# Optimization experiments

Hardware: AMD Instinct MI355X
Metric: run time of the kernel (lower is better)

The kernel has to match this reference:

```python
import jax, jax.numpy as jnp
import numpy as np

WIN = 8
SHIFT = WIN // 2  # shift=True
NH = 12
HD = 32
EPS = 1e-5


def _rel_pos_index(w):
    coords = np.stack(np.meshgrid(np.arange(w), np.arange(w), indexing='ij')).reshape(2, -1)
    rel = (coords[:, :, None] - coords[:, None, :]).transpose(1, 2, 0)
    rel[..., 0] += w - 1
    rel[..., 1] += w - 1
    rel[..., 0] *= 2 * w - 1
    return rel.sum(-1)  # [w*w, w*w]

REL_IDX = jnp.asarray(_rel_pos_index(WIN), dtype=jnp.int32)


def _ln(x, g, b):
    mu = jnp.mean(x, axis=-1, keepdims=True)
    var = jnp.mean(jnp.square(x - mu), axis=-1, keepdims=True)
    return (x - mu) * jax.lax.rsqrt(var + EPS) * g + b


def setup_inputs() -> dict:
    key = jax.random.key(0)
    ks = jax.random.split(key, 8)
    B, Hh, Ww, C = 16, 64, 64, 384
    s = lambda fan: 1.0 / np.sqrt(fan)
    return {
        'x': jax.random.normal(ks[0], (B, Hh * Ww, C), jnp.float32),
        'norm1_g': jnp.ones((C,), jnp.float32),
        'norm1_b': jnp.zeros((C,), jnp.float32),
        'qkv_w': jax.random.normal(ks[1], (3 * C, C), jnp.float32) * s(C),
        'qkv_b': jnp.zeros((3 * C,), jnp.float32),
        'proj_w': jax.random.normal(ks[2], (C, C), jnp.float32) * s(C),
        'proj_b': jnp.zeros((C,), jnp.float32),
        'rpb_table': jax.random.normal(ks[3], ((2 * WIN - 1) ** 2, NH), jnp.float32) * 0.02,
        'norm2_g': jnp.ones((C,), jnp.float32),
        'norm2_b': jnp.zeros((C,), jnp.float32),
        'fc1_w': jax.random.normal(ks[4], (4 * C, C), jnp.float32) * s(C),
        'fc1_b': jnp.zeros((4 * C,), jnp.float32),
        'fc2_w': jax.random.normal(ks[5], (C, 4 * C), jnp.float32) * s(4 * C),
        'fc2_b': jnp.zeros((C,), jnp.float32),
        'H': Hh,
        'W': Ww,
    }


def reference(x, norm1_g, norm1_b, qkv_w, qkv_b, proj_w, proj_b, rpb_table,
              norm2_g, norm2_b, fc1_w, fc1_b, fc2_w, fc2_b, H, W):
    B, N, C = x.shape
    Nw = WIN * WIN
    shortcut = x
    h = _ln(x, norm1_g, norm1_b)

    # window partition with roll (shifted windows)
    h = h.reshape(B, H, W, C)
    h = jnp.roll(h, shift=(-SHIFT, -SHIFT), axis=(1, 2))
    h = h.reshape(B, H // WIN, WIN, W // WIN, WIN, C).transpose(0, 1, 3, 2, 4, 5)
    h = h.reshape(-1, Nw, C)  # [B*nW, 64, C]

    # window attention
    qkv = h @ qkv_w.T + qkv_b  # [Bw, Nw, 3C]
    qkv = qkv.reshape(-1, Nw, 3, NH, HD).transpose(2, 0, 3, 1, 4)
    q, k, v = qkv[0], qkv[1], qkv[2]  # [Bw, NH, Nw, HD]
    attn = jnp.einsum('bhqd,bhkd->bhqk', q, k) * (HD ** -0.5)
    bias = rpb_table[REL_IDX.reshape(-1)].reshape(Nw, Nw, NH).transpose(2, 0, 1)
    attn = jax.nn.softmax(attn + bias[None], axis=-1)
    o = jnp.einsum('bhqk,bhkd->bhqd', attn, v)
    o = o.transpose(0, 2, 1, 3).reshape(-1, Nw, C)
    o = o @ proj_w.T + proj_b

    # window reverse with inverse roll
    o = o.reshape(B, H // WIN, W // WIN, WIN, WIN, C).transpose(0, 1, 3, 2, 4, 5)
    o = o.reshape(B, H, W, C)
    o = jnp.roll(o, shift=(SHIFT, SHIFT), axis=(1, 2)).reshape(B, N, C)

    x = shortcut + o
    m = _ln(x, norm2_g, norm2_b)
    m = jax.nn.gelu(m @ fc1_w.T + fc1_b, approximate=False)
    m = m @ fc2_w.T + fc2_b
    return x + m
```

## Files before the change

kernel.cpp:

```cpp
#include <hip/hip_runtime.h>
#include <hip/hip_bf16.h>
#include <math.h>

typedef __attribute__((ext_vector_type(8))) short bf16x8;
typedef __attribute__((ext_vector_type(4))) float f32x4;
typedef unsigned short u16;

#define NHEAD 12

__device__ __forceinline__ u16 f2bf(float f) {
  __hip_bfloat16 h = __float2bfloat16(f);
  return __builtin_bit_cast(u16, h);
}

__device__ __forceinline__ void gload16(const void* g, void* l) {
  __builtin_amdgcn_global_load_lds(
      (const __attribute__((address_space(1))) void*)g,
      (__attribute__((address_space(3))) void*)l, 16, 0, 0);
}

__global__ void cvt_all(const float* __restrict__ s0, const float* __restrict__ s1,
                        const float* __restrict__ s2, const float* __restrict__ s3,
                        u16* __restrict__ d) {
  int i = blockIdx.x * 256 + threadIdx.x;
  if (i >= 1769472) return;
  float v;
  if (i < 442368) v = s0[i];
  else if (i < 589824) v = s1[i - 442368];
  else if (i < 1179648) v = s2[i - 589824];
  else v = s3[i - 1179648];
  d[i] = f2bf(v);
}

__global__ void build_bias(const float* __restrict__ rpb, float* __restrict__ bt) {
  int i = blockIdx.x * 256 + threadIdx.x;
  if (i >= NHEAD * 4096) return;
  int h = i >> 12;
  int q = (i >> 6) & 63;
  int k = i & 63;
  int qi = q >> 3, qj = q & 7, ki = k >> 3, kj = k & 7;
  int idx = (qi - ki + 7) * 15 + (qj - kj + 7);
  bt[i] = rpb[idx * NHEAD + h];
}

__global__ __launch_bounds__(256) void ln_k(const float* __restrict__ x,
                                            const float* __restrict__ g,
                                            const float* __restrict__ b,
                                            u16* __restrict__ out) {
  int row = (blockIdx.x << 2) + (threadIdx.x >> 6);
  int lane = threadIdx.x & 63;
  const float* xr = x + (size_t)row * 384;
  float v[6];
  float s = 0.f;
#pragma unroll
  for (int i = 0; i < 6; ++i) { v[i] = xr[lane + (i << 6)]; s += v[i]; }
#pragma unroll
  for (int o = 32; o; o >>= 1) s += __shfl_xor(s, o, 64);
  float mu = s * (1.f / 384.f);
  float vs = 0.f;
#pragma unroll
  for (int i = 0; i < 6; ++i) { float d0 = v[i] - mu; vs += d0 * d0; }
#pragma unroll
  for (int o = 32; o; o >>= 1) vs += __shfl_xor(vs, o, 64);
  float rs = rsqrtf(vs * (1.f / 384.f) + 1e-5f);
  u16* orow = out + (size_t)row * 384;
#pragma unroll
  for (int i = 0; i < 6; ++i) {
    int c = lane + (i << 6);
    orow[c] = f2bf((v[i] - mu) * rs * g[c] + b[c]);
  }
}

template <int EP>
__global__ __launch_bounds__(256, 4) void gemmA(const u16* __restrict__ A,
                                                const u16* __restrict__ W,
                                                const float* __restrict__ bias,
                                                const float* __restrict__ res,
                                                void* __restrict__ outp,
                                                int N, int K, int nCol) {
  __shared__ u16 As[128 * 64];
  __shared__ u16 Bs[128 * 64];
  const int tid = threadIdx.x;
  const int wave = tid >> 6, lane = tid & 63;
  const int wm = wave >> 1, wn = wave & 1;
  const int nwg = gridDim.x, cpx = nwg >> 3;
  const int lin = (blockIdx.x & 7) * cpx + (blockIdx.x >> 3);
  const int rowT = lin / nCol;
  const int colT = lin - rowT * nCol;
  const int rowBase = rowT << 7;
  const int colBase = colT << 7;
  const int nK = K >> 6;

  const int g16 = (tid & 7) ^ ((tid >> 3) & 7);
  const u16* Asrc = A + (size_t)(rowBase + (tid >> 3)) * K + (g16 << 3);
  const u16* Wsrc = W + (size_t)(colBase + (tid >> 3)) * K + (g16 << 3);
  const int ldst = tid << 3;

  const int q4 = lane >> 4;
  const int rx = lane & 7;
  const int arow = (wm << 6) + (lane & 15);
  const int brow = (wn << 6) + (lane & 15);

  f32x4 acc[4][4] = {};

  for (int j = 0; j < nK; ++j) {
    const size_t k0 = (size_t)j << 6;
#pragma unroll
    for (int c = 0; c < 4; ++c) {
      gload16(Asrc + (size_t)(c << 5) * K + k0, &As[(c << 11) + ldst]);
      gload16(Wsrc + (size_t)(c << 5) * K + k0, &Bs[(c << 11) + ldst]);
    }
    __syncthreads();
#pragma unroll
    for (int kk = 0; kk < 2; ++kk) {
      const int slot = (((kk << 2) + q4) ^ rx) << 3;
      bf16x8 aF[4], bF[4];
#pragma unroll
      for (int m = 0; m < 4; ++m)
        aF[m] = *(const bf16x8*)&As[(arow + (m << 4)) * 64 + slot];
#pragma unroll
      for (int n = 0; n < 4; ++n)
        bF[n] = *(const bf16x8*)&Bs[(brow + (n << 4)) * 64 + slot];
#pragma unroll
      for (int m = 0; m < 4; ++m)
#pragma unroll
        for (int n = 0; n < 4; ++n)
          acc[m][n] = __builtin_amdgcn_mfma_f32_16x16x32_bf16(aF[m], bF[n], acc[m][n], 0, 0, 0);
    }
    __syncthreads();
  }

#pragma unroll
  for (int m = 0; m < 4; ++m) {
#pragma unroll
    for (int n = 0; n < 4; ++n) {
      const int col = colBase + (wn << 6) + (n << 4) + (lane & 15);
      const int row0 = rowBase + (wm << 6) + (m << 4) + ((lane >> 4) << 2);
      const float bv = bias[col];
#pragma unroll
      for (int jj = 0; jj < 4; ++jj) {
        const size_t row = (size_t)(row0 + jj);
        float y = acc[m][n][jj] + bv;
        if (EP == 0) {
          ((u16*)outp)[row * N + col] = f2bf(y);
        } else if (EP == 1) {
          ((float*)outp)[row * N + col] = y + res[row * N + col];
        } else if (EP == 2) {
          float y2 = y * y;
          float t = __builtin_fmaf(y2, 0.1029434f, 2.3022118f);
          float e = __builtin_amdgcn_exp2f(-(y * t));
          y = y * __builtin_amdgcn_rcpf(1.f + e);
          ((u16*)outp)[row * N + col] = f2bf(y);
        } else {
          ((float*)outp)[row * N + col] = y + res[row * N + col];
        }
      }
    }
  }
}

__global__ __launch_bounds__(256) void attn_k(const u16* __restrict__ qkv,
                                              const float* __restrict__ bias_tab,
                                              u16* __restrict__ o) {
  const int cpx = gridDim.x >> 3;
  const int lin = (blockIdx.x & 7) * cpx + (blockIdx.x >> 3);
  const int w = lin / NHEAD;
  const int h = lin - w * NHEAD;
  const int tid = threadIdx.x, wave = tid >> 6, lane = tid & 63;
  __shared__ u16 q_s[64 * 32];
  __shared__ u16 k_s[64 * 32];
  __shared__ u16 vt_s[32 * 64];
  __shared__ u16 p_s[4][16 * 72];
  const int b = w >> 6;
  const int wim = w & 63;
  const int wr0 = (wim >> 3) << 3, wc0 = (wim & 7) << 3;
  {
    const int r = tid >> 2, d0 = (tid & 3) << 3;
    const int pr = r >> 3, pc = r & 7;
    const int orow = (wr0 + pr + 4) & 63, ocol = (wc0 + pc + 4) & 63;
    const size_t t = ((size_t)b << 12) + (orow << 6) + ocol;
    const u16* base = qkv + t * 1152 + h * 32 + d0;
    *(uint4*)&q_s[r * 32 + d0] = *(const uint4*)(base);
    *(uint4*)&k_s[r * 32 + d0] = *(const uint4*)(base + 384);
    u16 vv[8];
    *(uint4*)vv = *(const uint4*)(base + 768);
#pragma unroll
    for (int j = 0; j < 8; ++j) vt_s[(d0 + j) * 64 + r] = vv[j];
  }
  __syncthreads();
  const int cIdx = lane & 15, rgrp = lane >> 4;
  const f32x4 zz = {0.f, 0.f, 0.f, 0.f};
  bf16x8 qa = *(const bf16x8*)&q_s[((wave << 4) + cIdx) * 32 + (rgrp << 3)];
  f32x4 s_acc[4];
#pragma unroll
  for (int n = 0; n < 4; ++n) {
    bf16x8 kb = *(const bf16x8*)&k_s[((n << 4) + cIdx) * 32 + (rgrp << 3)];
    s_acc[n] = __builtin_amdgcn_mfma_f32_16x16x32_bf16(qa, kb, zz, 0, 0, 0);
  }
  const float scale = 0.1767766952966369f;
  float mrow[4] = {-1e30f, -1e30f, -1e30f, -1e30f};
  const float* bt = bias_tab + h * 4096 + ((wave << 4) + (rgrp << 2)) * 64 + cIdx;
#pragma unroll
  for (int n = 0; n < 4; ++n)
#pragma unroll
    for (int j = 0; j < 4; ++j) {
      float val = s_acc[n][j] * scale + bt[j * 64 + (n << 4)];
      s_acc[n][j] = val;
      mrow[j] = fmaxf(mrow[j], val);
    }
#pragma unroll
  for (int j = 0; j < 4; ++j)
#pragma unroll
    for (int o2 = 1; o2 < 16; o2 <<= 1) mrow[j] = fmaxf(mrow[j], __shfl_xor(mrow[j], o2, 64));
  float srow[4] = {0.f, 0.f, 0.f, 0.f};
#pragma unroll
  for (int n = 0; n < 4; ++n)
#pragma unroll
    for (int j = 0; j < 4; ++j) {
      float e = __expf(s_acc[n][j] - mrow[j]);
      s_acc[n][j] = e;
      srow[j] += e;
    }
#pragma unroll
  for (int j = 0; j < 4; ++j)
#pragma unroll
    for (int o2 = 1; o2 < 16; o2 <<= 1) srow[j] += __shfl_xor(srow[j], o2, 64);
  float rinv[4];
#pragma unroll
  for (int j = 0; j < 4; ++j) rinv[j] = 1.f / srow[j];
  u16* pw = p_s[wave];
#pragma unroll
  for (int n = 0; n < 4; ++n)
#pragma unroll
    for (int j = 0; j < 4; ++j)
      pw[((rgrp << 2) + j) * 72 + (n << 4) + cIdx] = f2bf(s_acc[n][j] * rinv[j]);
  f32x4 o_acc[2] = {};
#pragma unroll
  for (int kk = 0; kk < 2; ++kk) {
    bf16x8 pa = *(const bf16x8*)&pw[cIdx * 72 + (kk << 5) + (rgrp << 3)];
#pragma unroll
    for (int c2 = 0; c2 < 2; ++c2) {
      bf16x8 vb = *(const bf16x8*)&vt_s[((c2 << 4) + cIdx) * 64 + (kk << 5) + (rgrp << 3)];
      o_acc[c2] = __builtin_amdgcn_mfma_f32_16x16x32_bf16(pa, vb, o_acc[c2], 0, 0, 0);
    }
  }
#pragma unroll
  for (int c2 = 0; c2 < 2; ++c2)
#pragma unroll
    for (int j = 0; j < 4; ++j) {
      const int p = (wave << 4) + (rgrp << 2) + j;
      const int pr = p >> 3, pc = p & 7;
      const int orow = (wr0 + pr + 4) & 63, ocol = (wc0 + pc + 4) & 63;
      const size_t t = ((size_t)b << 12) + (orow << 6) + ocol;
      o[t * 384 + h * 32 + (c2 << 4) + cIdx] = f2bf(o_acc[c2][j]);
    }
}

extern "C" void kernel_launch(void* const* d_in, const int* in_sizes, int n_in,
                              void* d_out, int out_size, void* d_ws, size_t ws_size,
                              hipStream_t stream) {
  const float* x = (const float*)d_in[0];
  const float* n1g = (const float*)d_in[1];
  const float* n1b = (const float*)d_in[2];
  const float* qkv_w = (const float*)d_in[3];
  const float* qkv_b = (const float*)d_in[4];
  const float* proj_w = (const float*)d_in[5];
  const float* proj_b = (const float*)d_in[6];
  const float* rpb = (const float*)d_in[7];
  const float* n2g = (const float*)d_in[8];
  const float* n2b = (const float*)d_in[9];
  const float* fc1_w = (const float*)d_in[10];
  const float* fc1_b = (const float*)d_in[11];
  const float* fc2_w = (const float*)d_in[12];
  const float* fc2_b = (const float*)d_in[13];

  char* ws = (char*)d_ws;
  u16* wqkv = (u16*)(ws + 0);
  u16* wproj = (u16*)(ws + 884736);
  u16* wfc1 = (u16*)(ws + 1179648);
  u16* wfc2 = (u16*)(ws + 2359296);
  float* bias_tab = (float*)(ws + 3538944);
  u16* qkv = (u16*)(ws + 3735552);
  u16* m1 = qkv;
  u16* hbuf = (u16*)(ws + 205062144);
  u16* obuf = hbuf;
  float* x1 = (float*)d_out;

  cvt_all<<<(1769472 + 255) / 256, 256, 0, stream>>>(qkv_w, proj_w, fc1_w, fc2_w, wqkv);
  build_bias<<<192, 256, 0, stream>>>(rpb, bias_tab);

  ln_k<<<16384, 256, 0, stream>>>(x, n1g, n1b, hbuf);
  gemmA<0><<<4608, 256, 0, stream>>>(hbuf, wqkv, qkv_b, nullptr, qkv, 1152, 384, 9);
  attn_k<<<12288, 256, 0, stream>>>(qkv, bias_tab, obuf);
  gemmA<1><<<1536, 256, 0, stream>>>(obuf, wproj, proj_b, x, x1, 384, 384, 3);
  ln_k<<<16384, 256, 0, stream>>>(x1, n2g, n2b, hbuf);
  gemmA<2><<<6144, 256, 0, stream>>>(hbuf, wfc1, fc1_b, nullptr, m1, 1536, 384, 12);
  gemmA<3><<<1536, 256, 0, stream>>>(m1, wfc2, fc2_b, x1, (float*)d_out, 384, 1536, 3);
}
```

Baseline: 476.6 us.

## Write QKV in window-major head layout and fuse proj GEMM with LayerNorm2

```diff
diff --git a/kernel.cpp b/kernel.cpp
--- a/kernel.cpp
+++ b/kernel.cpp
@@ -7,6 +7,8 @@
 typedef unsigned short u16;
 
 #define NHEAD 12
+#define MATS 25165824
+#define HEADS 2097152
 
 __device__ __forceinline__ u16 f2bf(float f) {
   __hip_bfloat16 h = __float2bfloat16(f);
@@ -130,36 +132,167 @@
     __syncthreads();
   }
 
-#pragma unroll
-  for (int m = 0; m < 4; ++m) {
+  float bv[4];
+#pragma unroll
+  for (int n = 0; n < 4; ++n) bv[n] = bias[colBase + (wn << 6) + (n << 4) + (lane & 15)];
+
+  if (EP == 0) {
+    int cp[4];
 #pragma unroll
     for (int n = 0; n < 4; ++n) {
-      const int col = colBase + (wn << 6) + (n << 4) + (lane & 15);
-      const int row0 = rowBase + (wm << 6) + (m << 4) + ((lane >> 4) << 2);
-      const float bv = bias[col];
+      int col = colBase + (wn << 6) + (n << 4) + (lane & 15);
+      int mat = (col >= 768) ? 2 : (col >= 384 ? 1 : 0);
+      int c = col - mat * 384;
+      cp[n] = mat * MATS + (c >> 5) * HEADS + (c & 31);
+    }
+#pragma unroll
+    for (int m = 0; m < 4; ++m)
 #pragma unroll
       for (int jj = 0; jj < 4; ++jj) {
-        const size_t row = (size_t)(row0 + jj);
-        float y = acc[m][n][jj] + bv;
-        if (EP == 0) {
-          ((u16*)outp)[row * N + col] = f2bf(y);
-        } else if (EP == 1) {
-          ((float*)outp)[row * N + col] = y + res[row * N + col];
-        } else if (EP == 2) {
-          float y2 = y * y;
-          float t = __builtin_fmaf(y2, 0.1029434f, 2.3022118f);
-          float e = __builtin_amdgcn_exp2f(-(y * t));
-          y = y * __builtin_amdgcn_rcpf(1.f + e);
-          ((u16*)outp)[row * N + col] = f2bf(y);
-        } else {
-          ((float*)outp)[row * N + col] = y + res[row * N + col];
+        int row = rowBase + (wm << 6) + (m << 4) + ((lane >> 4) << 2) + jj;
+        int b = row >> 12, R = (row >> 6) & 63, C = row & 63;
+        int rt = (R + 60) & 63, ct = (C + 60) & 63;
+        int rowpart = (((b << 6) + ((rt >> 3) << 3) + (ct >> 3)) << 11) +
+                      ((((rt & 7) << 3) + (ct & 7)) << 5);
+#pragma unroll
+        for (int n = 0; n < 4; ++n)
+          ((u16*)outp)[cp[n] + rowpart] = f2bf(acc[m][n][jj] + bv[n]);
+      }
+  } else {
+#pragma unroll
+    for (int m = 0; m < 4; ++m) {
+#pragma unroll
+      for (int n = 0; n < 4; ++n) {
+        const int col = colBase + (wn << 6) + (n << 4) + (lane & 15);
+        const int row0 = rowBase + (wm << 6) + (m << 4) + ((lane >> 4) << 2);
+#pragma unroll
+        for (int jj = 0; jj < 4; ++jj) {
+          const size_t row = (size_t)(row0 + jj);
+          float y = acc[m][n][jj] + bv[n];
+          if (EP == 2) {
+            float y2 = y * y;
+            float t = __builtin_fmaf(y2, 0.1029434f, 2.3022118f);
+            float e = __builtin_amdgcn_exp2f(-(y * t));
+            y = y * __builtin_amdgcn_rcpf(1.f + e);
+            ((u16*)outp)[row * N + col] = f2bf(y);
+          } else {
+            ((float*)outp)[row * N + col] = y + res[row * N + col];
+          }
         }
       }
     }
   }
 }
 
-__global__ __launch_bounds__(256) void attn_k(const u16* __restrict__ qkv,
+__global__ __launch_bounds__(512, 4) void projln_k(const u16* __restrict__ A,
+                                                   const u16* __restrict__ W,
+                                                   const float* __restrict__ bias,
+                                                   const float* __restrict__ res,
+                                                   const float* __restrict__ g2,
+                                                   const float* __restrict__ b2,
+                                                   float* __restrict__ x1,
+                                                   u16* __restrict__ h2) {
+  __shared__ u16 As[64 * 64];
+  __shared__ u16 Ws[384 * 64];
+  __shared__ float red[2][2][4][32];
+  const int tid = threadIdx.x;
+  const int wave = tid >> 6, lane = tid & 63;
+  const int wm = wave >> 2, wn = wave & 3;
+  const int rowBase = blockIdx.x << 6;
+
+  const int g16 = (tid & 7) ^ ((tid >> 3) & 7);
+  const u16* Asrc = A + (size_t)(rowBase + (tid >> 3)) * 384 + (g16 << 3);
+  const u16* Wsrc = W + (size_t)(tid >> 3) * 384 + (g16 << 3);
+  const int ldst = tid << 3;
+  const int q4 = lane >> 4, rx = lane & 7;
+  const int arow = (wm << 5) + (lane & 15);
+  const int brow = wn * 96 + (lane & 15);
+
+  f32x4 acc[2][6] = {};
+
+  for (int j = 0; j < 6; ++j) {
+    const size_t k0 = (size_t)j << 6;
+    gload16(Asrc + k0, &As[ldst]);
+#pragma unroll
+    for (int c = 0; c < 6; ++c)
+      gload16(Wsrc + (size_t)(c << 6) * 384 + k0, &Ws[(c << 12) + ldst]);
+    __syncthreads();
+#pragma unroll
+    for (int kk = 0; kk < 2; ++kk) {
+      const int slot = (((kk << 2) + q4) ^ rx) << 3;
+      bf16x8 aF[2], bF[6];
+#pragma unroll
+      for (int m = 0; m < 2; ++m)
+        aF[m] = *(const bf16x8*)&As[(arow + (m << 4)) * 64 + slot];
+#pragma unroll
+      for (int n = 0; n < 6; ++n)
+        bF[n] = *(const bf16x8*)&Ws[(brow + (n << 4)) * 64 + slot];
+#pragma unroll
+      for (int m = 0; m < 2; ++m)
+#pragma unroll
+        for (int n = 0; n < 6; ++n)
+          acc[m][n] = __builtin_amdgcn_mfma_f32_16x16x32_bf16(aF[m], bF[n], acc[m][n], 0, 0, 0);
+    }
+    __syncthreads();
+  }
+
+  float bv[6], gv[6], b2v[6];
+#pragma unroll
+  for (int n = 0; n < 6; ++n) {
+    int col = wn * 96 + (n << 4) + (lane & 15);
+    bv[n] = bias[col]; gv[n] = g2[col]; b2v[n] = b2[col];
+  }
+#pragma unroll
+  for (int m = 0; m < 2; ++m) {
+#pragma unroll
+    for (int jj = 0; jj < 4; ++jj) {
+      int row = rowBase + (wm << 5) + (m << 4) + ((lane >> 4) << 2) + jj;
+      const float* rr = res + (size_t)row * 384 + wn * 96 + (lane & 15);
+      float s = 0.f, sq = 0.f;
+#pragma unroll
+      for (int n = 0; n < 6; ++n) {
+        float v = acc[m][n][jj] + bv[n] + rr[n << 4];
+        acc[m][n][jj] = v;
+        s += v; sq += v * v;
+      }
+#pragma unroll
+      for (int o2 = 1; o2 < 16; o2 <<= 1) {
+        s += __shfl_xor(s, o2, 64);
+        sq += __shfl_xor(sq, o2, 64);
+      }
+      if ((lane & 15) == 0) {
+        int rloc = (m << 4) + ((lane >> 4) << 2) + jj;
+        red[0][wm][wn][rloc] = s;
+        red[1][wm][wn][rloc] = sq;
+      }
+    }
+  }
+  __syncthreads();
+#pragma unroll
+  for (int m = 0; m < 2; ++m) {
+#pragma unroll
+    for (int jj = 0; jj < 4; ++jj) {
+      int rloc = (m << 4) + ((lane >> 4) << 2) + jj;
+      float s = red[0][wm][0][rloc] + red[0][wm][1][rloc] + red[0][wm][2][rloc] + red[0][wm][3][rloc];
+      float sq = red[1][wm][0][rloc] + red[1][wm][1][rloc] + red[1][wm][2][rloc] + red[1][wm][3][rloc];
+      float mu = s * (1.f / 384.f);
+      float var = sq * (1.f / 384.f) - mu * mu;
+      float rs = rsqrtf(var + 1e-5f);
+      int row = rowBase + (wm << 5) + (m << 4) + ((lane >> 4) << 2) + jj;
+      float* xr = x1 + (size_t)row * 384;
+      u16* hr = h2 + (size_t)row * 384;
+      int cb = wn * 96 + (lane & 15);
+#pragma unroll
+      for (int n = 0; n < 6; ++n) {
+        float v = acc[m][n][jj];
+        xr[cb + (n << 4)] = v;
+        hr[cb + (n << 4)] = f2bf((v - mu) * rs * gv[n] + b2v[n]);
+      }
+    }
+  }
+}
+
+__global__ __launch_bounds__(256) void attn_k(const u16* __restrict__ qkvp,
                                               const float* __restrict__ bias_tab,
                                               u16* __restrict__ o) {
   const int cpx = gridDim.x >> 3;
@@ -171,22 +304,17 @@
   __shared__ u16 k_s[64 * 32];
   __shared__ u16 vt_s[32 * 64];
   __shared__ u16 p_s[4][16 * 72];
-  const int b = w >> 6;
-  const int wim = w & 63;
-  const int wr0 = (wim >> 3) << 3, wc0 = (wim & 7) << 3;
+  const u16* qb = qkvp + (size_t)h * HEADS + (w << 11);
+  gload16(qb + tid * 8, &q_s[tid * 8]);
+  gload16(qb + MATS + tid * 8, &k_s[tid * 8]);
   {
-    const int r = tid >> 2, d0 = (tid & 3) << 3;
-    const int pr = r >> 3, pc = r & 7;
-    const int orow = (wr0 + pr + 4) & 63, ocol = (wc0 + pc + 4) & 63;
-    const size_t t = ((size_t)b << 12) + (orow << 6) + ocol;
-    const u16* base = qkv + t * 1152 + h * 32 + d0;
-    *(uint4*)&q_s[r * 32 + d0] = *(const uint4*)(base);
-    *(uint4*)&k_s[r * 32 + d0] = *(const uint4*)(base + 384);
+    const int p = tid >> 2, d0 = (tid & 3) << 3;
     u16 vv[8];
-    *(uint4*)vv = *(const uint4*)(base + 768);
-#pragma unroll
-    for (int j = 0; j < 8; ++j) vt_s[(d0 + j) * 64 + r] = vv[j];
-  }
+    *(uint4*)vv = *(const uint4*)(qb + 2 * MATS + p * 32 + d0);
+#pragma unroll
+    for (int jj = 0; jj < 8; ++jj) vt_s[(d0 + jj) * 64 + p] = vv[jj];
+  }
+  asm volatile("s_waitcnt vmcnt(0)" ::: "memory");
   __syncthreads();
   const int cIdx = lane & 15, rgrp = lane >> 4;
   const f32x4 zz = {0.f, 0.f, 0.f, 0.f};
@@ -244,6 +372,9 @@
       o_acc[c2] = __builtin_amdgcn_mfma_f32_16x16x32_bf16(pa, vb, o_acc[c2], 0, 0, 0);
     }
   }
+  const int b = w >> 6;
+  const int wim = w & 63;
+  const int wr0 = (wim >> 3) << 3, wc0 = (wim & 7) << 3;
 #pragma unroll
   for (int c2 = 0; c2 < 2; ++c2)
 #pragma unroll
@@ -280,8 +411,8 @@
   u16* wfc1 = (u16*)(ws + 1179648);
   u16* wfc2 = (u16*)(ws + 2359296);
   float* bias_tab = (float*)(ws + 3538944);
-  u16* qkv = (u16*)(ws + 3735552);
-  u16* m1 = qkv;
+  u16* qkvp = (u16*)(ws + 3735552);
+  u16* m1 = qkvp;
   u16* hbuf = (u16*)(ws + 205062144);
   u16* obuf = hbuf;
   float* x1 = (float*)d_out;
@@ -290,10 +421,9 @@
   build_bias<<<192, 256, 0, stream>>>(rpb, bias_tab);
 
   ln_k<<<16384, 256, 0, stream>>>(x, n1g, n1b, hbuf);
-  gemmA<0><<<4608, 256, 0, stream>>>(hbuf, wqkv, qkv_b, nullptr, qkv, 1152, 384, 9);
-  attn_k<<<12288, 256, 0, stream>>>(qkv, bias_tab, obuf);
-  gemmA<1><<<1536, 256, 0, stream>>>(obuf, wproj, proj_b, x, x1, 384, 384, 3);
-  ln_k<<<16384, 256, 0, stream>>>(x1, n2g, n2b, hbuf);
+  gemmA<0><<<4608, 256, 0, stream>>>(hbuf, wqkv, qkv_b, nullptr, qkvp, 1152, 384, 9);
+  attn_k<<<12288, 256, 0, stream>>>(qkvp, bias_tab, obuf);
+  projln_k<<<1024, 512, 0, stream>>>(obuf, wproj, proj_b, x, n2g, n2b, x1, hbuf);
   gemmA<2><<<6144, 256, 0, stream>>>(hbuf, wfc1, fc1_b, nullptr, m1, 1536, 384, 12);
   gemmA<3><<<1536, 256, 0, stream>>>(m1, wfc2, fc2_b, x1, (float*)d_out, 384, 1536, 3);
 }
```

Result: slower. 492.0 us (+3.2%).

## Fuse projection GEMM with residual add and second LayerNorm

Applied to the files above, without the earlier changes.

```diff
diff --git a/kernel.cpp b/kernel.cpp
--- a/kernel.cpp
+++ b/kernel.cpp
@@ -143,8 +143,6 @@
         float y = acc[m][n][jj] + bv;
         if (EP == 0) {
           ((u16*)outp)[row * N + col] = f2bf(y);
-        } else if (EP == 1) {
-          ((float*)outp)[row * N + col] = y + res[row * N + col];
         } else if (EP == 2) {
           float y2 = y * y;
           float t = __builtin_fmaf(y2, 0.1029434f, 2.3022118f);
@@ -154,6 +152,113 @@
         } else {
           ((float*)outp)[row * N + col] = y + res[row * N + col];
         }
+      }
+    }
+  }
+}
+
+__global__ __launch_bounds__(512, 4) void projln_k(const u16* __restrict__ A,
+                                                   const u16* __restrict__ W,
+                                                   const float* __restrict__ bias,
+                                                   const float* __restrict__ res,
+                                                   const float* __restrict__ g2,
+                                                   const float* __restrict__ b2,
+                                                   float* __restrict__ x1,
+                                                   u16* __restrict__ h2) {
+  __shared__ u16 As[64 * 64];
+  __shared__ u16 Ws[384 * 64];
+  __shared__ float red[2][8][64];
+  const int tid = threadIdx.x;
+  const int wave = tid >> 6, lane = tid & 63;
+  const int nwg = gridDim.x, cpx = nwg >> 3;
+  const int lin = (blockIdx.x & 7) * cpx + (blockIdx.x >> 3);
+  const int rowBase = lin << 6;
+
+  const int g16 = (tid & 7) ^ ((tid >> 3) & 7);
+  const u16* Asrc = A + (size_t)(rowBase + (tid >> 3)) * 384 + (g16 << 3);
+  const u16* Wsrc = W + (size_t)(tid >> 3) * 384 + (g16 << 3);
+  const int ldst = tid << 3;
+  const int q4 = lane >> 4, rx = lane & 7;
+  const int arow = lane & 15;
+  const int brow = wave * 48 + (lane & 15);
+
+  f32x4 acc[4][3] = {};
+
+  for (int j = 0; j < 6; ++j) {
+    const size_t k0 = (size_t)j << 6;
+    gload16(Asrc + k0, &As[ldst & 8191]);
+#pragma unroll
+    for (int c = 0; c < 6; ++c)
+      gload16(Wsrc + (size_t)(c << 6) * 384 + k0, &Ws[(c << 12) + ldst]);
+    __syncthreads();
+#pragma unroll
+    for (int kk = 0; kk < 2; ++kk) {
+      const int slot = (((kk << 2) + q4) ^ rx) << 3;
+      bf16x8 aF[4], bF[3];
+#pragma unroll
+      for (int m = 0; m < 4; ++m)
+        aF[m] = *(const bf16x8*)&As[(arow + (m << 4)) * 64 + slot];
+#pragma unroll
+      for (int n = 0; n < 3; ++n)
+        bF[n] = *(const bf16x8*)&Ws[(brow + (n << 4)) * 64 + slot];
+#pragma unroll
+      for (int m = 0; m < 4; ++m)
+#pragma unroll
+        for (int n = 0; n < 3; ++n)
+          acc[m][n] = __builtin_amdgcn_mfma_f32_16x16x32_bf16(aF[m], bF[n], acc[m][n], 0, 0, 0);
+    }
+    __syncthreads();
+  }
+
+  float bv[3], gv[3], b2v[3];
+#pragma unroll
+  for (int n = 0; n < 3; ++n) {
+    int col = wave * 48 + (n << 4) + (lane & 15);
+    bv[n] = bias[col]; gv[n] = g2[col]; b2v[n] = b2[col];
+  }
+#pragma unroll
+  for (int m = 0; m < 4; ++m) {
+#pragma unroll
+    for (int jj = 0; jj < 4; ++jj) {
+      const int rl = (m << 4) + (q4 << 2) + jj;
+      const int row = rowBase + rl;
+      const float* rr = res + (size_t)row * 384 + wave * 48 + (lane & 15);
+      float s = 0.f, sq = 0.f;
+#pragma unroll
+      for (int n = 0; n < 3; ++n) {
+        float v = acc[m][n][jj] + bv[n] + rr[n << 4];
+        acc[m][n][jj] = v;
+        s += v; sq += v * v;
+      }
+#pragma unroll
+      for (int o2 = 1; o2 < 16; o2 <<= 1) {
+        s += __shfl_xor(s, o2, 64);
+        sq += __shfl_xor(sq, o2, 64);
+      }
+      if ((lane & 15) == 0) { red[0][wave][rl] = s; red[1][wave][rl] = sq; }
+    }
+  }
+  __syncthreads();
+#pragma unroll
+  for (int m = 0; m < 4; ++m) {
+#pragma unroll
+    for (int jj = 0; jj < 4; ++jj) {
+      const int rl = (m << 4) + (q4 << 2) + jj;
+      float s = 0.f, sq = 0.f;
+#pragma unroll
+      for (int wv = 0; wv < 8; ++wv) { s += red[0][wv][rl]; sq += red[1][wv][rl]; }
+      float mu = s * (1.f / 384.f);
+      float var = sq * (1.f / 384.f) - mu * mu;
+      float rs = rsqrtf(var + 1e-5f);
+      const int row = rowBase + rl;
+      float* xr = x1 + (size_t)row * 384;
+      u16* hr = h2 + (size_t)row * 384;
+#pragma unroll
+      for (int n = 0; n < 3; ++n) {
+        int c = wave * 48 + (n << 4) + (lane & 15);
+        float v = acc[m][n][jj];
+        xr[c] = v;
+        hr[c] = f2bf((v - mu) * rs * gv[n] + b2v[n]);
       }
     }
   }
@@ -292,8 +397,7 @@
   ln_k<<<16384, 256, 0, stream>>>(x, n1g, n1b, hbuf);
   gemmA<0><<<4608, 256, 0, stream>>>(hbuf, wqkv, qkv_b, nullptr, qkv, 1152, 384, 9);
   attn_k<<<12288, 256, 0, stream>>>(qkv, bias_tab, obuf);
-  gemmA<1><<<1536, 256, 0, stream>>>(obuf, wproj, proj_b, x, x1, 384, 384, 3);
-  ln_k<<<16384, 256, 0, stream>>>(x1, n2g, n2b, hbuf);
+  projln_k<<<1024, 512, 0, stream>>>(obuf, wproj, proj_b, x, n2g, n2b, x1, hbuf);
   gemmA<2><<<6144, 256, 0, stream>>>(hbuf, wfc1, fc1_b, nullptr, m1, 1536, 384, 12);
   gemmA<3><<<1536, 256, 0, stream>>>(m1, wfc2, fc2_b, x1, (float*)d_out, 384, 1536, 3);
 }
```

New measurement: 489.8 us. 1.03x slower.
